# Performance work log

Hardware: AMD Instinct MI355X
Metric: run time of the kernel (lower is better)

## Reference

```python
import jax, jax.numpy as jnp
from jax import lax
import numpy as np

B, N, M, C, K = 2, 16384, 4096, 16, 32
RADIUS = 0.1
EPS = 1e-8


def setup_inputs() -> dict:
    key = jax.random.key(0)
    ks = jax.random.split(key, 9)
    return {
        "xyz": jax.random.uniform(ks[0], (B, N, 3), jnp.float32),
        "new_xyz": jax.random.uniform(ks[1], (B, M, 3), jnp.float32),
        "features": jax.random.normal(ks[2], (B, C, N), jnp.float32),
        "w0": jax.random.normal(ks[3], (32, C), jnp.float32) * 0.1,
        "b0": jax.random.normal(ks[4], (32,), jnp.float32) * 0.1,
        "w1": jax.random.normal(ks[5], (64, 32), jnp.float32) * 0.1,
        "b1": jax.random.normal(ks[6], (64,), jnp.float32) * 0.1,
        "wxyz": jax.random.normal(ks[7], (32, 3), jnp.float32) * 0.1,
        "bxyz": jax.random.normal(ks[8], (32,), jnp.float32) * 0.1,
    }


def ball_query(xyz, new_xyz, radius, nsample):
    """Return (idx [B,M,K] int32, idn multiplicity [B,M,K] int32, has_any [B,M] bool).
    Matches pointnet2 ball_query: first `nsample` in-radius indices (ascending),
    empty slots padded with the first found index; idn counts how many times an
    index is duplicated in a row (0 everywhere for rows with no neighbor)."""
    d2 = jnp.sum((new_xyz[:, :, None, :] - xyz[:, None, :, :]) ** 2, axis=-1)  # B,M,N
    n = xyz.shape[1]
    score = jnp.where(d2 < radius * radius,
                      jnp.arange(n, dtype=jnp.int32), jnp.int32(n))
    idx = -lax.top_k(-score, nsample)[0]          # B,M,K smallest indices, asc
    valid = idx < n
    idx = jnp.where(valid, idx, idx[..., :1])      # pad with first found index
    has_any = valid[..., 0]
    idx = jnp.where(idx >= n, 0, idx)              # safe gather for empty rows
    cnt = jnp.sum(idx[..., :, None] == idx[..., None, :], axis=-1).astype(jnp.int32)
    idn = jnp.where(has_any[..., None], cnt, 0)
    return idx, idn, has_any


def reference(xyz, new_xyz, features, w0, b0, w1, b1, wxyz, bxyz):
    idx, idn, has_any = ball_query(xyz, new_xyz, RADIUS, K)
    b_idx = jnp.arange(xyz.shape[0])[:, None, None]
    # QueryAndGroup: relative coords + gathered features
    rel = xyz[b_idx, idx] - new_xyz[:, :, None, :]            # B,M,K,3
    rel = jnp.transpose(rel, (0, 3, 1, 2))                    # B,3,M,K
    gfeat = jnp.transpose(features, (0, 2, 1))[b_idx, idx]    # B,M,K,C
    gfeat = jnp.transpose(gfeat, (0, 3, 1, 2))                # B,C,M,K

    # distance-reciprocal weights, duplicate-corrected by idn, row-normalized
    dist = jnp.linalg.norm(rel, axis=1, keepdims=True)        # B,1,M,K
    dist_recip = 1.0 / (dist + EPS)
    _idn = jnp.where(has_any[:, None, :, None], idn[:, None, :, :], 1).astype(dist.dtype)
    dist_recip = dist_recip / _idn
    weights = dist_recip / jnp.sum(dist_recip, axis=3, keepdims=True)
    idn_mask = has_any[:, None, :, None].astype(dist.dtype)
    weights = weights * idn_mask                              # zero empty rows

    # SharedMLP on features: 1x1 conv == per-point matmul, ReLU
    h = jax.nn.relu(jnp.einsum('bcmk,oc->bomk', gfeat, w0) + b0[None, :, None, None])
    h = jax.nn.relu(jnp.einsum('bcmk,oc->bomk', h, w1) + b1[None, :, None, None])
    feat_sum = jnp.sum(weights * h, axis=3)                   # B,64,M weighted sum-pool

    # xyz branch: SharedMLP [3,32] + max-pool over neighbors
    hx = jax.nn.relu(jnp.einsum('bcmk,oc->bomk', rel, wxyz) + bxyz[None, :, None, None])
    feat_max = jnp.max(hx, axis=3)                            # B,32,M

    return new_xyz, jnp.concatenate([feat_max, feat_sum], axis=1)  # (B,M,3),(B,96,M)
```

## Files before the change

kernel.cpp:

```cpp
#include <hip/hip_runtime.h>
#include <math.h>
#include <limits.h>

#define BB 2
#define NN 16384
#define MM 4096
#define CCH 16
#define KK 32
#define R2 0.01f
#define EPSV 1e-8f
#define GD 10
#define CPB (GD*GD*GD)
#define CAP 56
#define NCELL (BB*CPB)
#define WSA_OFF 8192
#define WSB_OFF 10240
#define BUCKET_OFF 16384
#define WS_GRID (BUCKET_OFF + (size_t)NCELL*CAP*16)
#define NDW 512

typedef __attribute__((ext_vector_type(8))) short short8;
typedef __attribute__((ext_vector_type(4))) float v4f;

__device__ __forceinline__ short f2bf(float f) {
    unsigned u = __float_as_uint(f);
    unsigned r = u + 0x7FFFu + ((u >> 16) & 1u);
    return (short)(r >> 16);
}
__device__ __forceinline__ unsigned pk2(float a, float b) {
    return (unsigned)(unsigned short)f2bf(a) | ((unsigned)(unsigned short)f2bf(b) << 16);
}

__device__ __forceinline__ int cell_of(float x, float y, float z) {
    int cx = min(GD-1, max(0, (int)(x * 10.0f)));
    int cy = min(GD-1, max(0, (int)(y * 10.0f)));
    int cz = min(GD-1, max(0, (int)(z * 10.0f)));
    return (cx*GD + cy)*GD + cz;
}

__global__ void k_scatter(const float* __restrict__ xyz,
                          const float* __restrict__ w0, const float* __restrict__ w1,
                          int* __restrict__ cnt, int* __restrict__ ovf,
                          float4* __restrict__ buckets,
                          short8* __restrict__ wsA, short8* __restrict__ wsB) {
    if (blockIdx.x == 0) {
        int t = threadIdx.x;
        if (t < 128) {
            int fi = t >> 6, l = t & 63, l15 = l & 15, qd = (l >> 4) & 3;
            short8 a = {0,0,0,0,0,0,0,0};
            if (qd < 2)
                #pragma unroll
                for (int j = 0; j < 8; ++j)
                    a[j] = f2bf(w0[(fi*16 + l15)*CCH + qd*8 + j]);
            wsA[fi*64 + l] = a;
        }
        if (t < 64) {
            int l15 = t & 15, qd = t >> 4;
            #pragma unroll
            for (int u = 0; u < 4; ++u) {
                const float* wr = w1 + ((u << 4) + l15)*32 + (qd << 3);
                short8 bb;
                #pragma unroll
                for (int j = 0; j < 8; ++j) bb[j] = f2bf(wr[j]);
                wsB[t*4 + u] = bb;
            }
        }
    }
    int i = blockIdx.x*256 + threadIdx.x;
    if (i >= BB*NN) return;
    const float* p = xyz + (size_t)i*3;
    int b = i >> 14;
    int n = i & (NN-1);
    float x = p[0], y = p[1], z = p[2];
    int cell = b*CPB + cell_of(x, y, z);
    int slot = atomicAdd(&cnt[cell], 1);
    if (slot < CAP)
        buckets[(size_t)cell*CAP + slot] = make_float4(x, y, z, __int_as_float(n));
    else
        *ovf = 1;
}

__global__ __launch_bounds__(256, 4) void grouper_fused(
    const float* __restrict__ xyz, const float* __restrict__ new_xyz,
    const float* __restrict__ feat,
    const float* __restrict__ w0, const float* __restrict__ b0,
    const float* __restrict__ w1, const float* __restrict__ b1,
    const float* __restrict__ wxyz, const float* __restrict__ bxyz,
    const int* __restrict__ cnt, const int* __restrict__ ovf,
    const float4* __restrict__ buckets,
    const short8* __restrict__ wsA, const short8* __restrict__ wsB,
    int use_grid,
    float* __restrict__ out)
{
    const int lane = threadIdx.x & 63;
    const int wid  = threadIdx.x >> 6;
    const int q    = (blockIdx.x << 2) + wid;
    const int b    = q >> 12;
    const int m    = q & (MM - 1);

    __shared__ int s_idx[4][KK];
    __shared__ float4 s_rel[4][KK];
    __shared__ __align__(16) unsigned s_bm[4][NDW];
    __shared__ __align__(16) short s_h0t[4][32*32];

    const float* xb = xyz + (size_t)b * NN * 3;
    const float qx = new_xyz[((size_t)b*MM + m)*3 + 0];
    const float qy = new_xyz[((size_t)b*MM + m)*3 + 1];
    const float qz = new_xyz[((size_t)b*MM + m)*3 + 2];
    const unsigned long long below = (1ull << lane) - 1ull;

    int nfound = 0, idx0 = 0;
    bool need_full = (use_grid == 0) || (use_grid && ovf[0] != 0);

    if (!need_full) {
        uint4 z4 = make_uint4(0u, 0u, 0u, 0u);
        *(uint4*)&s_bm[wid][lane*8]     = z4;
        *(uint4*)&s_bm[wid][lane*8 + 4] = z4;

        int x0 = max(0, (int)floorf((qx - 0.1f)*10.0f - 1e-3f));
        int x1 = min(GD-1, (int)floorf((qx + 0.1f)*10.0f + 1e-3f));
        int y0 = max(0, (int)floorf((qy - 0.1f)*10.0f - 1e-3f));
        int y1 = min(GD-1, (int)floorf((qy + 0.1f)*10.0f + 1e-3f));
        int z0 = max(0, (int)floorf((qz - 0.1f)*10.0f - 1e-3f));
        int z1 = min(GD-1, (int)floorf((qz + 0.1f)*10.0f + 1e-3f));

        int myCell = -1, ncells = 0;
        int myCx = 0, myCy = 0, myCz = 0;
        for (int cx = x0; cx <= x1; ++cx)
        for (int cy = y0; cy <= y1; ++cy)
        for (int cz = z0; cz <= z1; ++cz) {
            if (lane == ncells) {
                myCell = b*CPB + (cx*GD + cy)*GD + cz;
                myCx = cx; myCy = cy; myCz = cz;
            }
            ++ncells;
        }
        int myCnt = 0, myBase = 0;
        if (myCell >= 0) {
            float xlo = myCx*0.1f, ylo = myCy*0.1f, zlo = myCz*0.1f;
            float ddx = fmaxf(fmaxf(xlo - qx, qx - (xlo + 0.1f)), 0.0f);
            float ddy = fmaxf(fmaxf(ylo - qy, qy - (ylo + 0.1f)), 0.0f);
            float ddz = fmaxf(fmaxf(zlo - qz, qz - (zlo + 0.1f)), 0.0f);
            if (ddx*ddx + ddy*ddy + ddz*ddz < R2) {
                myCnt = min(cnt[myCell], CAP);
                myBase = myCell*CAP;
            }
        }

        __builtin_amdgcn_wave_barrier();

        int cc0 = __builtin_amdgcn_readlane(myCnt, 0);
        int cb0 = __builtin_amdgcn_readlane(myBase, 0);
        float4 p0 = make_float4(0.f, 0.f, 0.f, 0.f);
        if (lane < cc0) p0 = buckets[cb0 + lane];
        for (int c = 0; c < ncells; ++c) {
            int cc1 = 0, cb1 = 0;
            if (c + 1 < ncells) {
                cc1 = __builtin_amdgcn_readlane(myCnt, c + 1);
                cb1 = __builtin_amdgcn_readlane(myBase, c + 1);
            }
            float4 pn = make_float4(0.f, 0.f, 0.f, 0.f);
            if (lane < cc1) pn = buckets[cb1 + lane];
            if (lane < cc0) {
                float dx = p0.x - qx, dy = p0.y - qy, dz = p0.z - qz;
                float d2 = dx*dx + dy*dy + dz*dz;
                if (d2 < R2) {
                    int id = __float_as_int(p0.w);
                    atomicOr(&s_bm[wid][id >> 5], 1u << (id & 31));
                }
            }
            cc0 = cc1; cb0 = cb1; p0 = pn;
        }

        __builtin_amdgcn_wave_barrier();

        uint4 d0 = *(uint4*)&s_bm[wid][lane*8];
        uint4 d1 = *(uint4*)&s_bm[wid][lane*8 + 4];
        unsigned dw[8] = {d0.x, d0.y, d0.z, d0.w, d1.x, d1.y, d1.z, d1.w};
        int pc = 0;
        #pragma unroll
        for (int j = 0; j < 8; ++j) pc += __popc(dw[j]);
        int pre = pc;
        #pragma unroll
        for (int d = 1; d < 64; d <<= 1) {
            int t = __shfl_up(pre, d);
            if (lane >= d) pre += t;
        }
        int total = __shfl(pre, 63);
        int rank = pre - pc;
        nfound = min(total, KK);

        if (rank < KK) {
            #pragma unroll
            for (int j = 0; j < 8; ++j) {
                unsigned bits = dw[j];
                while (bits && rank < KK) {
                    int bpos = __builtin_ctz(bits);
                    s_idx[wid][rank] = ((lane*8 + j) << 5) + bpos;
                    bits &= bits - 1;
                    ++rank;
                }
            }
        }

        __builtin_amdgcn_wave_barrier();
        idx0 = (nfound > 0) ? s_idx[wid][0] : 0;
        __builtin_amdgcn_wave_barrier();
        if (lane >= nfound && lane < KK) s_idx[wid][lane] = idx0;
        __builtin_amdgcn_wave_barrier();
    }

    if (need_full) {
        int cntf = 0;
        for (int basep = 0; basep < NN; basep += 256) {
            float d2a[4];
            #pragma unroll
            for (int j = 0; j < 4; ++j) {
                int i = basep + (j << 6) + lane;
                float px = xb[i*3+0], py = xb[i*3+1], pz = xb[i*3+2];
                float dx = px - qx, dy = py - qy, dz = pz - qz;
                d2a[j] = dx*dx + dy*dy + dz*dz;
            }
            #pragma unroll
            for (int j = 0; j < 4; ++j) {
                bool hit = d2a[j] < R2;
                unsigned long long msk = __ballot(hit);
                if (hit) {
                    int pos = cntf + __popcll(msk & below);
                    if (pos < KK) s_idx[wid][pos] = basep + (j << 6) + lane;
                }
                cntf += __popcll(msk);
            }
            if (cntf >= KK) break;
        }
        nfound = cntf < KK ? cntf : KK;
        __builtin_amdgcn_wave_barrier();
        if (lane < KK) {
            int v = 0;
            if (nfound > 0) v = (lane < nfound) ? s_idx[wid][lane] : s_idx[wid][0];
            s_idx[wid][lane] = v;
        }
        __builtin_amdgcn_wave_barrier();
        idx0 = s_idx[wid][0];
    }

    {
        const int k = lane & 31;
        const int h = lane >> 5;
        const int ik = s_idx[wid][k];
        float px = xb[ik*3+0], py = xb[ik*3+1], pz = xb[ik*3+2];
        float rx = px - qx, ry = py - qy, rz = pz - qz;
        float dist = sqrtf(rx*rx + ry*ry + rz*rz);
        float recip = 1.0f / (dist + EPSV);
        float mult = (float)(1 + KK - nfound);
        float w = recip / ((ik == idx0) ? mult : 1.0f);
        float S = w;
        #pragma unroll
        for (int d = 1; d < 32; d <<= 1) S += __shfl_xor(S, d);
        float wk = (nfound > 0) ? (w / S) : 0.0f;
        if (h == 0) s_rel[wid][k] = make_float4(rx, ry, rz, wk);
    }
    __builtin_amdgcn_wave_barrier();

    const int l15 = lane & 15;
    const int quad = lane >> 4;

    short8 A1, A1b, Bf[4];
    if (use_grid) {
        A1  = wsA[lane];
        A1b = wsA[64 + lane];
        #pragma unroll
        for (int u = 0; u < 4; ++u) Bf[u] = wsB[lane*4 + u];
    } else {
        short8 z = {0,0,0,0,0,0,0,0};
        A1 = z; A1b = z;
        if (quad < 2) {
            #pragma unroll
            for (int j = 0; j < 8; ++j) {
                A1[j]  = f2bf(w0[l15*CCH + quad*8 + j]);
                A1b[j] = f2bf(w0[(16 + l15)*CCH + quad*8 + j]);
            }
        }
        #pragma unroll
        for (int u = 0; u < 4; ++u) {
            const float* wr = w1 + ((u << 4) + l15)*32 + (quad << 3);
            #pragma unroll
            for (int j = 0; j < 8; ++j) Bf[u][j] = f2bf(wr[j]);
        }
    }

    short8 G0 = {0,0,0,0,0,0,0,0}, G1 = {0,0,0,0,0,0,0,0};
    {
        const float* fb = feat + (size_t)b * CCH * NN;
        if (quad < 2) {
            int ika = s_idx[wid][l15];
            int ikb = s_idx[wid][16 + l15];
            int cb0 = quad << 3;
            #pragma unroll
            for (int j = 0; j < 8; ++j) {
                G0[j] = f2bf(fb[(cb0 + j)*NN + ika]);
                G1[j] = f2bf(fb[(cb0 + j)*NN + ikb]);
            }
        }
    }

    v4f C0, C1;
    #pragma unroll
    for (int r = 0; r < 4; ++r) {
        C0[r] = b0[(quad << 2) + r];
        C1[r] = b0[16 + (quad << 2) + r];
    }

    v4f H00 = __builtin_amdgcn_mfma_f32_16x16x32_bf16(A1,  G0, C0, 0, 0, 0);
    v4f H01 = __builtin_amdgcn_mfma_f32_16x16x32_bf16(A1b, G0, C1, 0, 0, 0);
    v4f H10 = __builtin_amdgcn_mfma_f32_16x16x32_bf16(A1,  G1, C0, 0, 0, 0);
    v4f H11 = __builtin_amdgcn_mfma_f32_16x16x32_bf16(A1b, G1, C1, 0, 0, 0);

    short* hb = &s_h0t[wid][0];
    {
        uint2 w;
        w.x = pk2(fmaxf(H00[0],0.f), fmaxf(H00[1],0.f));
        w.y = pk2(fmaxf(H00[2],0.f), fmaxf(H00[3],0.f));
        *(uint2*)&hb[l15*32 + (quad << 2)] = w;
        w.x = pk2(fmaxf(H01[0],0.f), fmaxf(H01[1],0.f));
        w.y = pk2(fmaxf(H01[2],0.f), fmaxf(H01[3],0.f));
        *(uint2*)&hb[l15*32 + 16 + (quad << 2)] = w;
        w.x = pk2(fmaxf(H10[0],0.f), fmaxf(H10[1],0.f));
        w.y = pk2(fmaxf(H10[2],0.f), fmaxf(H10[3],0.f));
        *(uint2*)&hb[(16 + l15)*32 + (quad << 2)] = w;
        w.x = pk2(fmaxf(H11[0],0.f), fmaxf(H11[1],0.f));
        w.y = pk2(fmaxf(H11[2],0.f), fmaxf(H11[3],0.f));
        *(uint2*)&hb[(16 + l15)*32 + 16 + (quad << 2)] = w;
    }
    __builtin_amdgcn_wave_barrier();

    short8 A2_0 = *(short8*)&hb[l15*32 + (quad << 3)];
    short8 A2_1 = *(short8*)&hb[(16 + l15)*32 + (quad << 3)];

    float wkv[2][4];
    #pragma unroll
    for (int t = 0; t < 2; ++t)
        #pragma unroll
        for (int r = 0; r < 4; ++r)
            wkv[t][r] = s_rel[wid][16*t + (quad << 2) + r].w;

    float* out2 = out + (size_t)BB*MM*3 + (size_t)b*96*MM;

    float Su[4];
    #pragma unroll
    for (int u = 0; u < 4; ++u) {
        float b1u = b1[(u << 4) + l15];
        v4f Cb = {b1u, b1u, b1u, b1u};
        v4f D0 = __builtin_amdgcn_mfma_f32_16x16x32_bf16(A2_0, Bf[u], Cb, 0, 0, 0);
        v4f D1 = __builtin_amdgcn_mfma_f32_16x16x32_bf16(A2_1, Bf[u], Cb, 0, 0, 0);
        float s = 0.f;
        #pragma unroll
        for (int r = 0; r < 4; ++r)
            s += wkv[0][r]*fmaxf(D0[r], 0.f) + wkv[1][r]*fmaxf(D1[r], 0.f);
        s += __shfl_xor(s, 16);
        s += __shfl_xor(s, 32);
        Su[u] = s;
    }
    float sout = (quad == 0) ? Su[0] : (quad == 1) ? Su[1] : (quad == 2) ? Su[2] : Su[3];
    out2[(32 + lane)*MM + m] = sout;

    {
        const int c = lane & 31;
        const int h = lane >> 5;
        const float wx0 = wxyz[c*3+0], wx1 = wxyz[c*3+1], wx2 = wxyz[c*3+2];
        const float bc = bxyz[c];
        float v = 0.0f;
        #pragma unroll
        for (int kk = 0; kk < 16; ++kk) {
            float4 hr = s_rel[wid][(h << 4) + kk];
            float t = bc + wx0*hr.x + wx1*hr.y + wx2*hr.z;
            v = fmaxf(v, fmaxf(t, 0.0f));
        }
        v = fmaxf(v, __shfl_xor(v, 32));
        if (h == 0) out2[c*MM + m] = v;
    }

    if (lane == 0) {
        float* o0 = out + ((size_t)b*MM + m)*3;
        o0[0] = qx; o0[1] = qy; o0[2] = qz;
    }
}

extern "C" void kernel_launch(void* const* d_in, const int* in_sizes, int n_in,
                              void* d_out, int out_size, void* d_ws, size_t ws_size,
                              hipStream_t stream) {
    const float* xyz     = (const float*)d_in[0];
    const float* new_xyz = (const float*)d_in[1];
    const float* feat    = (const float*)d_in[2];
    const float* w0      = (const float*)d_in[3];
    const float* b0      = (const float*)d_in[4];
    const float* w1      = (const float*)d_in[5];
    const float* b1      = (const float*)d_in[6];
    const float* wxyz    = (const float*)d_in[7];
    const float* bxyz    = (const float*)d_in[8];
    float* out = (float*)d_out;

    int* ovf = (int*)d_ws;
    int* cnt = (int*)((char*)d_ws + 64);
    short8* wsA = (short8*)((char*)d_ws + WSA_OFF);
    short8* wsB = (short8*)((char*)d_ws + WSB_OFF);
    float4* buckets = (float4*)((char*)d_ws + BUCKET_OFF);
    const int use_grid = (d_ws != nullptr && ws_size >= WS_GRID) ? 1 : 0;

    if (use_grid) {
        hipMemsetAsync(d_ws, 0, BUCKET_OFF, stream);
        hipLaunchKernelGGL(k_scatter, dim3((BB*NN+255)/256), dim3(256), 0, stream,
                           xyz, w0, w1, cnt, ovf, buckets, wsA, wsB);
    }
    hipLaunchKernelGGL(grouper_fused, dim3((BB*MM)/4), dim3(256), 0, stream,
                       xyz, new_xyz, feat, w0, b0, w1, b1, wxyz, bxyz,
                       cnt, ovf, buckets, wsA, wsB, use_grid, out);
}
```

Before: 115.9 us.

## Compact grid-cell candidates into a flat table and scan all lanes densely

Replaces the per-cell loop, where each iteration processed one cell's points with many lanes idle, with a wave-wide prefix sum that builds a flat shared-memory table of bucket slots. All 64 lanes then stream through candidates densely, so fewer iterations are needed. Cell coordinates are now computed directly per lane instead of through a serial triple loop. The shared buffer is reused for the hidden activations with a padded row stride to reduce LDS bank conflicts. Rows with more than 768 candidates fall back to the full scan.

```diff
diff --git a/kernel.cpp b/kernel.cpp
--- a/kernel.cpp
+++ b/kernel.cpp
@@ -18,6 +18,8 @@
 #define BUCKET_OFF 16384
 #define WS_GRID (BUCKET_OFF + (size_t)NCELL*CAP*16)
 #define NDW 512
+#define TBL 768
+#define HST 40
 
 typedef __attribute__((ext_vector_type(8))) short short8;
 typedef __attribute__((ext_vector_type(4))) float v4f;
@@ -101,7 +103,7 @@
     __shared__ int s_idx[4][KK];
     __shared__ float4 s_rel[4][KK];
     __shared__ __align__(16) unsigned s_bm[4][NDW];
-    __shared__ __align__(16) short s_h0t[4][32*32];
+    __shared__ __align__(16) int s_tbl[4][TBL];
 
     const float* xb = xyz + (size_t)b * NN * 3;
     const float qx = new_xyz[((size_t)b*MM + m)*3 + 0];
@@ -124,90 +126,104 @@
         int z0 = max(0, (int)floorf((qz - 0.1f)*10.0f - 1e-3f));
         int z1 = min(GD-1, (int)floorf((qz + 0.1f)*10.0f + 1e-3f));
 
-        int myCell = -1, ncells = 0;
-        int myCx = 0, myCy = 0, myCz = 0;
-        for (int cx = x0; cx <= x1; ++cx)
-        for (int cy = y0; cy <= y1; ++cy)
-        for (int cz = z0; cz <= z1; ++cz) {
-            if (lane == ncells) {
-                myCell = b*CPB + (cx*GD + cy)*GD + cz;
-                myCx = cx; myCy = cy; myCz = cz;
-            }
-            ++ncells;
-        }
+        const int nzc = z1 - z0 + 1, nyc = y1 - y0 + 1, nxc = x1 - x0 + 1;
+        const int nyz = nyc * nzc;
+        const int ncells = nxc * nyz;
         int myCnt = 0, myBase = 0;
-        if (myCell >= 0) {
-            float xlo = myCx*0.1f, ylo = myCy*0.1f, zlo = myCz*0.1f;
+        if (lane < ncells) {
+            const float rnyz = 1.0f / (float)nyz;
+            const float rnz  = 1.0f / (float)nzc;
+            int cxr = (int)((float)lane * rnyz + 1e-4f);
+            int rem = lane - cxr * nyz;
+            int cyr = (int)((float)rem * rnz + 1e-4f);
+            int czr = rem - cyr * nzc;
+            int cx = x0 + cxr, cy = y0 + cyr, cz = z0 + czr;
+            float xlo = cx*0.1f, ylo = cy*0.1f, zlo = cz*0.1f;
             float ddx = fmaxf(fmaxf(xlo - qx, qx - (xlo + 0.1f)), 0.0f);
             float ddy = fmaxf(fmaxf(ylo - qy, qy - (ylo + 0.1f)), 0.0f);
             float ddz = fmaxf(fmaxf(zlo - qz, qz - (zlo + 0.1f)), 0.0f);
             if (ddx*ddx + ddy*ddy + ddz*ddz < R2) {
-                myCnt = min(cnt[myCell], CAP);
-                myBase = myCell*CAP;
-            }
-        }
-
-        __builtin_amdgcn_wave_barrier();
-
-        int cc0 = __builtin_amdgcn_readlane(myCnt, 0);
-        int cb0 = __builtin_amdgcn_readlane(myBase, 0);
-        float4 p0 = make_float4(0.f, 0.f, 0.f, 0.f);
-        if (lane < cc0) p0 = buckets[cb0 + lane];
-        for (int c = 0; c < ncells; ++c) {
-            int cc1 = 0, cb1 = 0;
-            if (c + 1 < ncells) {
-                cc1 = __builtin_amdgcn_readlane(myCnt, c + 1);
-                cb1 = __builtin_amdgcn_readlane(myBase, c + 1);
-            }
-            float4 pn = make_float4(0.f, 0.f, 0.f, 0.f);
-            if (lane < cc1) pn = buckets[cb1 + lane];
-            if (lane < cc0) {
-                float dx = p0.x - qx, dy = p0.y - qy, dz = p0.z - qz;
-                float d2 = dx*dx + dy*dy + dz*dz;
-                if (d2 < R2) {
-                    int id = __float_as_int(p0.w);
-                    atomicOr(&s_bm[wid][id >> 5], 1u << (id & 31));
+                int cell = b*CPB + (cx*GD + cy)*GD + cz;
+                myCnt = min(cnt[cell], CAP);
+                myBase = cell*CAP;
+            }
+        }
+
+        int incl = myCnt;
+        #pragma unroll
+        for (int d = 1; d < 64; d <<= 1) {
+            int t = __shfl_up(incl, d);
+            if (lane >= d) incl += t;
+        }
+        const int total = __shfl(incl, 63);
+        const int wbase = incl - myCnt;
+
+        if (total > TBL) {
+            need_full = true;
+        } else {
+            int* tbl = &s_tbl[wid][0];
+            for (int t = 0; t < myCnt; ++t) tbl[wbase + t] = myBase + t;
+            __builtin_amdgcn_wave_barrier();
+
+            const int iters = (total + 63) >> 6;
+            int j = lane;
+            bool v0 = (j < total);
+            int sl0 = v0 ? tbl[j] : 0;
+            float4 p0 = make_float4(0.f, 0.f, 0.f, 0.f);
+            if (v0) p0 = buckets[sl0];
+            for (int it = 0; it < iters; ++it) {
+                int jn = j + 64;
+                bool v1 = (jn < total);
+                int sl1 = v1 ? tbl[jn] : 0;
+                float4 pn = make_float4(0.f, 0.f, 0.f, 0.f);
+                if (v1) pn = buckets[sl1];
+                if (v0) {
+                    float dx = p0.x - qx, dy = p0.y - qy, dz = p0.z - qz;
+                    if (dx*dx + dy*dy + dz*dz < R2) {
+                        int id = __float_as_int(p0.w);
+                        atomicOr(&s_bm[wid][id >> 5], 1u << (id & 31));
+                    }
                 }
-            }
-            cc0 = cc1; cb0 = cb1; p0 = pn;
-        }
-
-        __builtin_amdgcn_wave_barrier();
-
-        uint4 d0 = *(uint4*)&s_bm[wid][lane*8];
-        uint4 d1 = *(uint4*)&s_bm[wid][lane*8 + 4];
-        unsigned dw[8] = {d0.x, d0.y, d0.z, d0.w, d1.x, d1.y, d1.z, d1.w};
-        int pc = 0;
-        #pragma unroll
-        for (int j = 0; j < 8; ++j) pc += __popc(dw[j]);
-        int pre = pc;
-        #pragma unroll
-        for (int d = 1; d < 64; d <<= 1) {
-            int t = __shfl_up(pre, d);
-            if (lane >= d) pre += t;
-        }
-        int total = __shfl(pre, 63);
-        int rank = pre - pc;
-        nfound = min(total, KK);
-
-        if (rank < KK) {
-            #pragma unroll
-            for (int j = 0; j < 8; ++j) {
-                unsigned bits = dw[j];
-                while (bits && rank < KK) {
-                    int bpos = __builtin_ctz(bits);
-                    s_idx[wid][rank] = ((lane*8 + j) << 5) + bpos;
-                    bits &= bits - 1;
-                    ++rank;
+                j = jn; v0 = v1; sl0 = sl1; p0 = pn;
+            }
+
+            __builtin_amdgcn_wave_barrier();
+
+            uint4 d0 = *(uint4*)&s_bm[wid][lane*8];
+            uint4 d1 = *(uint4*)&s_bm[wid][lane*8 + 4];
+            unsigned dw[8] = {d0.x, d0.y, d0.z, d0.w, d1.x, d1.y, d1.z, d1.w};
+            int pc = 0;
+            #pragma unroll
+            for (int jj = 0; jj < 8; ++jj) pc += __popc(dw[jj]);
+            int pre = pc;
+            #pragma unroll
+            for (int d = 1; d < 64; d <<= 1) {
+                int t = __shfl_up(pre, d);
+                if (lane >= d) pre += t;
+            }
+            int tt = __shfl(pre, 63);
+            int rank = pre - pc;
+            nfound = min(tt, KK);
+
+            if (rank < KK) {
+                #pragma unroll
+                for (int jj = 0; jj < 8; ++jj) {
+                    unsigned bits = dw[jj];
+                    while (bits && rank < KK) {
+                        int bpos = __builtin_ctz(bits);
+                        s_idx[wid][rank] = ((lane*8 + jj) << 5) + bpos;
+                        bits &= bits - 1;
+                        ++rank;
+                    }
                 }
             }
-        }
-
-        __builtin_amdgcn_wave_barrier();
-        idx0 = (nfound > 0) ? s_idx[wid][0] : 0;
-        __builtin_amdgcn_wave_barrier();
-        if (lane >= nfound && lane < KK) s_idx[wid][lane] = idx0;
-        __builtin_amdgcn_wave_barrier();
+
+            __builtin_amdgcn_wave_barrier();
+            idx0 = (nfound > 0) ? s_idx[wid][0] : 0;
+            __builtin_amdgcn_wave_barrier();
+            if (lane >= nfound && lane < KK) s_idx[wid][lane] = idx0;
+            __builtin_amdgcn_wave_barrier();
+        }
     }
 
     if (need_full) {
@@ -316,26 +332,27 @@
     v4f H10 = __builtin_amdgcn_mfma_f32_16x16x32_bf16(A1,  G1, C0, 0, 0, 0);
     v4f H11 = __builtin_amdgcn_mfma_f32_16x16x32_bf16(A1b, G1, C1, 0, 0, 0);
 
-    short* hb = &s_h0t[wid][0];
+    __builtin_amdgcn_wave_barrier();
+    short* hb = (short*)&s_tbl[wid][0];
     {
         uint2 w;
         w.x = pk2(fmaxf(H00[0],0.f), fmaxf(H00[1],0.f));
         w.y = pk2(fmaxf(H00[2],0.f), fmaxf(H00[3],0.f));
-        *(uint2*)&hb[l15*32 + (quad << 2)] = w;
+        *(uint2*)&hb[l15*HST + (quad << 2)] = w;
         w.x = pk2(fmaxf(H01[0],0.f), fmaxf(H01[1],0.f));
         w.y = pk2(fmaxf(H01[2],0.f), fmaxf(H01[3],0.f));
-        *(uint2*)&hb[l15*32 + 16 + (quad << 2)] = w;
+        *(uint2*)&hb[l15*HST + 16 + (quad << 2)] = w;
         w.x = pk2(fmaxf(H10[0],0.f), fmaxf(H10[1],0.f));
         w.y = pk2(fmaxf(H10[2],0.f), fmaxf(H10[3],0.f));
-        *(uint2*)&hb[(16 + l15)*32 + (quad << 2)] = w;
+        *(uint2*)&hb[(16 + l15)*HST + (quad << 2)] = w;
         w.x = pk2(fmaxf(H11[0],0.f), fmaxf(H11[1],0.f));
         w.y = pk2(fmaxf(H11[2],0.f), fmaxf(H11[3],0.f));
-        *(uint2*)&hb[(16 + l15)*32 + 16 + (quad << 2)] = w;
+        *(uint2*)&hb[(16 + l15)*HST + 16 + (quad << 2)] = w;
     }
     __builtin_amdgcn_wave_barrier();
 
-    short8 A2_0 = *(short8*)&hb[l15*32 + (quad << 3)];
-    short8 A2_1 = *(short8*)&hb[(16 + l15)*32 + (quad << 3)];
+    short8 A2_0 = *(short8*)&hb[l15*HST + (quad << 3)];
+    short8 A2_1 = *(short8*)&hb[(16 + l15)*HST + (quad << 3)];
 
     float wkv[2][4];
     #pragma unroll
```

Measured after the change: 108.6 us. 1.07x faster.
